# Performance work log

Measured on AMD Instinct MI355X. Metric: run time of the kernel, lower is better.

## Reference

```python
import jax, jax.numpy as jnp
import numpy as np

STRIDES = (8, 16, 32, 64, 128)
THRESHOLD = 0.5
B, C = 8, 80
HS = (160, 80, 40, 20, 10)


def setup_inputs() -> dict:
    key = jax.random.key(0)
    ks = jax.random.split(key, 3 * len(HS))
    d = {}
    for i, h in enumerate(HS):
        d[f"cls_{i}"] = jax.random.normal(ks[3 * i], (B, C, h, h), jnp.float32)
        d[f"bbox_{i}"] = jax.random.normal(ks[3 * i + 1], (B, 4, h, h), jnp.float32)
        d[f"ctr_{i}"] = jax.random.normal(ks[3 * i + 2], (B, 1, h, h), jnp.float32)
    return d


def _filter_level(cls, bbox, ctr, stride, thr):
    # cls: [B,C,H,W], bbox: [B,4,H,W], ctr: [B,1,H,W] (NCHW, as asserted in source)
    b, c, h, w = cls.shape
    scores = cls.transpose(0, 2, 3, 1).reshape(b, h * w, c)   # [B,HW,C]
    bboxes = bbox.transpose(0, 2, 3, 1).reshape(b, h * w, 4)  # [B,HW,4]
    ctrs = ctr.transpose(0, 2, 3, 1).reshape(b, h * w, 1)     # [B,HW,1]
    # FilterModule keeps locations whose max class score exceeds threshold.
    mask = (jnp.max(scores, axis=-1) > thr)[..., None].astype(scores.dtype)  # [B,HW,1]
    ys, xs = jnp.meshgrid(jnp.arange(h), jnp.arange(w), indexing="ij")
    half = stride // 2
    coord = jnp.stack([xs * stride + half, ys * stride + half], axis=-1)  # [H,W,2]
    coord = coord.reshape(h * w, 2).astype(scores.dtype)
    coord = jnp.broadcast_to(coord, (b, h * w, 2))
    # Static-shape compaction: zero out non-selected locations instead of
    # producing dynamic-length per-image lists (jit-compatible equivalent of
    # the per-image coord/score/bbox/centerness gather).
    return jnp.concatenate(
        [coord * mask, scores * mask, bboxes * mask, ctrs * mask], axis=-1
    )  # [B, HW, 2 + C + 4 + 1]


def reference(cls_0, bbox_0, ctr_0, cls_1, bbox_1, ctr_1, cls_2, bbox_2, ctr_2,
              cls_3, bbox_3, ctr_3, cls_4, bbox_4, ctr_4):
    levels = [
        (cls_0, bbox_0, ctr_0),
        (cls_1, bbox_1, ctr_1),
        (cls_2, bbox_2, ctr_2),
        (cls_3, bbox_3, ctr_3),
        (cls_4, bbox_4, ctr_4),
    ]
    return tuple(
        _filter_level(c, bb, ct, s, THRESHOLD)
        for (c, bb, ct), s in zip(levels, STRIDES)
    )
```

## Files before the change

### kernel.cpp

```cpp
#include <hip/hip_runtime.h>

#define OUTCH 87
#define WPOS  8
#define WWORDS 704

typedef float f32x4 __attribute__((ext_vector_type(4)));

__global__ __launch_bounds__(256) void fcos_filter_kernel(
    const float* __restrict__ cl0, const float* __restrict__ bb0, const float* __restrict__ ct0,
    const float* __restrict__ cl1, const float* __restrict__ bb1, const float* __restrict__ ct1,
    const float* __restrict__ cl2, const float* __restrict__ bb2, const float* __restrict__ ct2,
    const float* __restrict__ cl3, const float* __restrict__ bb3, const float* __restrict__ ct3,
    const float* __restrict__ cl4, const float* __restrict__ bb4, const float* __restrict__ ct4,
    float* __restrict__ out)
{
    __shared__ float lds[4 * WWORDS];

    const int tid  = threadIdx.x;
    const int wv   = tid >> 6;
    const int lane = tid & 63;
    float* wlds  = lds + wv * WWORDS;
    float* wflag = wlds + 696;

    const int gw = blockIdx.x * 4 + wv;

    const float *cls, *bbx, *ctr;
    int img, wi, HW, W, str, ksh;
    size_t obase;
    if (gw < 25600)      { cls=cl0;bbx=bb0;ctr=ct0;HW=25600;W=160;str=8;  ksh=4;obase=0u;
                           img = gw / 3200;          wi = gw - img * 3200; }
    else if (gw < 32000) { cls=cl1;bbx=bb1;ctr=ct1;HW=6400; W=80; str=16; ksh=3;obase=17817600u;
                           const int t = gw - 25600; img = t / 800;  wi = t - img * 800; }
    else if (gw < 33600) { cls=cl2;bbx=bb2;ctr=ct2;HW=1600; W=40; str=32; ksh=2;obase=22272000u;
                           const int t = gw - 32000; img = t / 200;  wi = t - img * 200; }
    else if (gw < 34000) { cls=cl3;bbx=bb3;ctr=ct3;HW=400;  W=20; str=64; ksh=1;obase=23385600u;
                           const int t = gw - 33600; img = t / 50;   wi = t - img * 50; }
    else                 { cls=cl4;bbx=bb4;ctr=ct4;HW=100;  W=10; str=128;ksh=0;obase=23664000u;
                           const int t = gw - 34000; img = t / 13;   wi = t - img * 13; }

    const int p0    = wi * WPOS;
    const int valid = min(WPOS, HW - p0);

    const int  cb  = lane >> 1;
    const int  q   = lane & 1;
    const bool pok = (4 * q) < valid;
    const size_t posoff = (size_t)(p0 + 4 * q);

    float4 v0, v1, v2;
    float4 fm; fm.x = fm.y = fm.z = fm.w = -1e30f;
    if (pok) {
        const float* a0 = cls + ((size_t)img * 80 + cb) * HW + posoff;
        v0 = *reinterpret_cast<const float4*>(a0);
        v1 = *reinterpret_cast<const float4*>(a0 + (size_t)32 * HW);
        fm.x = fmaxf(v0.x, v1.x); fm.y = fmaxf(v0.y, v1.y);
        fm.z = fmaxf(v0.z, v1.z); fm.w = fmaxf(v0.w, v1.w);
    }
    const bool r2 = pok && (cb < 21);
    if (r2) {
        const int c = 64 + cb;
        const float* s = (c < 80) ? cls + ((size_t)img * 80 + c) * HW
                       : (c < 84) ? bbx + ((size_t)img * 4 + (c - 80)) * HW
                                  : ctr + (size_t)img * HW;
        v2 = *reinterpret_cast<const float4*>(s + posoff);
        if (cb < 16) {
            fm.x = fmaxf(fm.x, v2.x); fm.y = fmaxf(fm.y, v2.y);
            fm.z = fmaxf(fm.z, v2.z); fm.w = fmaxf(fm.w, v2.w);
        }
    }

    #pragma unroll
    for (int m = 2; m <= 32; m <<= 1) {
        fm.x = fmaxf(fm.x, __shfl_xor(fm.x, m));
        fm.y = fmaxf(fm.y, __shfl_xor(fm.y, m));
        fm.z = fmaxf(fm.z, __shfl_xor(fm.z, m));
        fm.w = fmaxf(fm.w, __shfl_xor(fm.w, m));
    }
    float4 mk;
    mk.x = (fm.x > 0.5f) ? 1.0f : 0.0f;
    mk.y = (fm.y > 0.5f) ? 1.0f : 0.0f;
    mk.z = (fm.z > 0.5f) ? 1.0f : 0.0f;
    mk.w = (fm.w > 0.5f) ? 1.0f : 0.0f;

    const int r0w = 4 * q * 87;
    if (pok) {
        wlds[r0w +   0 + 2 + cb]      = v0.x * mk.x;
        wlds[r0w +  87 + 2 + cb]      = v0.y * mk.y;
        wlds[r0w + 174 + 2 + cb]      = v0.z * mk.z;
        wlds[r0w + 261 + 2 + cb]      = v0.w * mk.w;
        wlds[r0w +   0 + 34 + cb]     = v1.x * mk.x;
        wlds[r0w +  87 + 34 + cb]     = v1.y * mk.y;
        wlds[r0w + 174 + 34 + cb]     = v1.z * mk.z;
        wlds[r0w + 261 + 34 + cb]     = v1.w * mk.w;
    }
    if (r2) {
        wlds[r0w +   0 + 66 + cb]     = v2.x * mk.x;
        wlds[r0w +  87 + 66 + cb]     = v2.y * mk.y;
        wlds[r0w + 174 + 66 + cb]     = v2.z * mk.z;
        wlds[r0w + 261 + 66 + cb]     = v2.w * mk.w;
    }
    if (lane < 2) {
        f32x4 mo; mo.x = mk.x; mo.y = mk.y; mo.z = mk.z; mo.w = mk.w;
        *reinterpret_cast<f32x4*>(wflag + 4 * lane) = mo;
    }
    if (lane < 8) {
        const float m = wflag[lane];
        const int pg = p0 + lane;
        const int t  = pg >> ksh;
        const int y  = t / 10;
        const int x  = pg - y * W;
        wlds[lane * 87 + 0] = (float)(x * str + (str >> 1)) * m;
        wlds[lane * 87 + 1] = (float)(y * str + (str >> 1)) * m;
    }

    float* dst = out + obase + ((size_t)img * HW + p0) * OUTCH;
    const int nw = valid * OUTCH;
    {
        const int w = 4 * lane;
        if (w < nw) *reinterpret_cast<f32x4*>(dst + w) = *reinterpret_cast<const f32x4*>(wlds + w);
    }
    {
        const int w = 4 * (lane + 64);
        if (w < nw) *reinterpret_cast<f32x4*>(dst + w) = *reinterpret_cast<const f32x4*>(wlds + w);
    }
    {
        const int w = 4 * (lane + 128);
        if (w < nw) *reinterpret_cast<f32x4*>(dst + w) = *reinterpret_cast<const f32x4*>(wlds + w);
    }
}

extern "C" void kernel_launch(void* const* d_in, const int* in_sizes, int n_in,
                              void* d_out, int out_size, void* d_ws, size_t ws_size,
                              hipStream_t stream) {
    (void)in_sizes; (void)n_in; (void)out_size; (void)d_ws; (void)ws_size;
    fcos_filter_kernel<<<8526, 256, 0, stream>>>(
        (const float*)d_in[0],  (const float*)d_in[1],  (const float*)d_in[2],
        (const float*)d_in[3],  (const float*)d_in[4],  (const float*)d_in[5],
        (const float*)d_in[6],  (const float*)d_in[7],  (const float*)d_in[8],
        (const float*)d_in[9],  (const float*)d_in[10], (const float*)d_in[11],
        (const float*)d_in[12], (const float*)d_in[13], (const float*)d_in[14],
        (float*)d_out);
}
```

Measured before the change: 34.98 us.

## Make kernel persistent with grid-stride tiles and prefetch next tile's loads

Launches a fixed grid of 2048 blocks where each wave walks tiles with a grid stride. The global loads for the next tile are issued before the current tile is processed, so load latency overlaps with the LDS transpose and the stores. Loads are now unconditional, using a clamped offset for invalid positions, to keep them hoistable. This costs extra registers and leaves the last iteration with nothing to overlap, and with fewer blocks in flight memory-level parallelism may drop.

```diff
diff --git a/kernel.cpp b/kernel.cpp
--- a/kernel.cpp
+++ b/kernel.cpp
@@ -1,72 +1,69 @@
 #include <hip/hip_runtime.h>
-
-#define OUTCH 87
-#define WPOS  8
-#define WWORDS 704
 
 typedef float f32x4 __attribute__((ext_vector_type(4)));
 
-__global__ __launch_bounds__(256) void fcos_filter_kernel(
-    const float* __restrict__ cl0, const float* __restrict__ bb0, const float* __restrict__ ct0,
-    const float* __restrict__ cl1, const float* __restrict__ bb1, const float* __restrict__ ct1,
-    const float* __restrict__ cl2, const float* __restrict__ bb2, const float* __restrict__ ct2,
-    const float* __restrict__ cl3, const float* __restrict__ bb3, const float* __restrict__ ct3,
-    const float* __restrict__ cl4, const float* __restrict__ bb4, const float* __restrict__ ct4,
-    float* __restrict__ out)
+#define NTILES  34104
+#define NWAVES  8192
+#define WWORDS  704
+
+struct Tile {
+    const float *cls, *bbx, *ctr;
+    int img, HW, W, str, ksh, p0, valid;
+    long obase;
+};
+
+__device__ __forceinline__ Tile decode(int gw,
+    const float* cl0, const float* bb0, const float* ct0,
+    const float* cl1, const float* bb1, const float* ct1,
+    const float* cl2, const float* bb2, const float* ct2,
+    const float* cl3, const float* bb3, const float* ct3,
+    const float* cl4, const float* bb4, const float* ct4)
 {
-    __shared__ float lds[4 * WWORDS];
+    Tile T; int wi;
+    if (gw < 25600)      { T.cls=cl0;T.bbx=bb0;T.ctr=ct0;T.HW=25600;T.W=160;T.str=8;  T.ksh=4;T.obase=0;
+                           T.img = gw / 3200;          wi = gw - T.img * 3200; }
+    else if (gw < 32000) { T.cls=cl1;T.bbx=bb1;T.ctr=ct1;T.HW=6400; T.W=80; T.str=16; T.ksh=3;T.obase=17817600;
+                           const int u = gw - 25600;   T.img = u / 800;  wi = u - T.img * 800; }
+    else if (gw < 33600) { T.cls=cl2;T.bbx=bb2;T.ctr=ct2;T.HW=1600; T.W=40; T.str=32; T.ksh=2;T.obase=22272000;
+                           const int u = gw - 32000;   T.img = u / 200;  wi = u - T.img * 200; }
+    else if (gw < 34000) { T.cls=cl3;T.bbx=bb3;T.ctr=ct3;T.HW=400;  T.W=20; T.str=64; T.ksh=1;T.obase=23385600;
+                           const int u = gw - 33600;   T.img = u / 50;   wi = u - T.img * 50; }
+    else                 { T.cls=cl4;T.bbx=bb4;T.ctr=ct4;T.HW=100;  T.W=10; T.str=128;T.ksh=0;T.obase=23664000;
+                           const int u = gw - 34000;   T.img = u / 13;   wi = u - T.img * 13; }
+    T.p0 = wi * 8;
+    T.valid = min(8, T.HW - T.p0);
+    return T;
+}
 
-    const int tid  = threadIdx.x;
-    const int wv   = tid >> 6;
-    const int lane = tid & 63;
-    float* wlds  = lds + wv * WWORDS;
-    float* wflag = wlds + 696;
+__device__ __forceinline__ void issue(const Tile& T, int cb, int q,
+                                      float4& v0, float4& v1, float4& v2)
+{
+    const int qo = (4 * q < T.valid) ? 4 * q : 0;
+    const size_t po = (size_t)(T.p0 + qo);
+    const float* a0 = T.cls + ((size_t)T.img * 80 + cb) * T.HW + po;
+    v0 = *reinterpret_cast<const float4*>(a0);
+    v1 = *reinterpret_cast<const float4*>(a0 + (size_t)32 * T.HW);
+    const int c = 64 + ((cb < 21) ? cb : 20);
+    const float* s = (c < 80) ? T.cls + ((size_t)T.img * 80 + c) * T.HW
+                   : (c < 84) ? T.bbx + ((size_t)T.img * 4 + (c - 80)) * T.HW
+                              : T.ctr + (size_t)T.img * T.HW;
+    v2 = *reinterpret_cast<const float4*>(s + po);
+}
 
-    const int gw = blockIdx.x * 4 + wv;
+__device__ __forceinline__ void process(const Tile& T, int lane, int cb, int q,
+                                        float* wlds, float* wflag, float* __restrict__ out,
+                                        const float4& v0, const float4& v1, const float4& v2)
+{
+    const bool pok = 4 * q < T.valid;
 
-    const float *cls, *bbx, *ctr;
-    int img, wi, HW, W, str, ksh;
-    size_t obase;
-    if (gw < 25600)      { cls=cl0;bbx=bb0;ctr=ct0;HW=25600;W=160;str=8;  ksh=4;obase=0u;
-                           img = gw / 3200;          wi = gw - img * 3200; }
-    else if (gw < 32000) { cls=cl1;bbx=bb1;ctr=ct1;HW=6400; W=80; str=16; ksh=3;obase=17817600u;
-                           const int t = gw - 25600; img = t / 800;  wi = t - img * 800; }
-    else if (gw < 33600) { cls=cl2;bbx=bb2;ctr=ct2;HW=1600; W=40; str=32; ksh=2;obase=22272000u;
-                           const int t = gw - 32000; img = t / 200;  wi = t - img * 200; }
-    else if (gw < 34000) { cls=cl3;bbx=bb3;ctr=ct3;HW=400;  W=20; str=64; ksh=1;obase=23385600u;
-                           const int t = gw - 33600; img = t / 50;   wi = t - img * 50; }
-    else                 { cls=cl4;bbx=bb4;ctr=ct4;HW=100;  W=10; str=128;ksh=0;obase=23664000u;
-                           const int t = gw - 34000; img = t / 13;   wi = t - img * 13; }
-
-    const int p0    = wi * WPOS;
-    const int valid = min(WPOS, HW - p0);
-
-    const int  cb  = lane >> 1;
-    const int  q   = lane & 1;
-    const bool pok = (4 * q) < valid;
-    const size_t posoff = (size_t)(p0 + 4 * q);
-
-    float4 v0, v1, v2;
-    float4 fm; fm.x = fm.y = fm.z = fm.w = -1e30f;
-    if (pok) {
-        const float* a0 = cls + ((size_t)img * 80 + cb) * HW + posoff;
-        v0 = *reinterpret_cast<const float4*>(a0);
-        v1 = *reinterpret_cast<const float4*>(a0 + (size_t)32 * HW);
-        fm.x = fmaxf(v0.x, v1.x); fm.y = fmaxf(v0.y, v1.y);
-        fm.z = fmaxf(v0.z, v1.z); fm.w = fmaxf(v0.w, v1.w);
+    float4 fm;
+    fm.x = fmaxf(v0.x, v1.x); fm.y = fmaxf(v0.y, v1.y);
+    fm.z = fmaxf(v0.z, v1.z); fm.w = fmaxf(v0.w, v1.w);
+    if (cb < 16) {
+        fm.x = fmaxf(fm.x, v2.x); fm.y = fmaxf(fm.y, v2.y);
+        fm.z = fmaxf(fm.z, v2.z); fm.w = fmaxf(fm.w, v2.w);
     }
-    const bool r2 = pok && (cb < 21);
-    if (r2) {
-        const int c = 64 + cb;
-        const float* s = (c < 80) ? cls + ((size_t)img * 80 + c) * HW
-                       : (c < 84) ? bbx + ((size_t)img * 4 + (c - 80)) * HW
-                                  : ctr + (size_t)img * HW;
-        v2 = *reinterpret_cast<const float4*>(s + posoff);
-        if (cb < 16) {
-            fm.x = fmaxf(fm.x, v2.x); fm.y = fmaxf(fm.y, v2.y);
-            fm.z = fmaxf(fm.z, v2.z); fm.w = fmaxf(fm.w, v2.w);
-        }
-    }
+    if (!pok) { fm.x = fm.y = fm.z = fm.w = -1e30f; }
 
     #pragma unroll
     for (int m = 2; m <= 32; m <<= 1) {
@@ -83,20 +80,20 @@
 
     const int r0w = 4 * q * 87;
     if (pok) {
-        wlds[r0w +   0 + 2 + cb]      = v0.x * mk.x;
-        wlds[r0w +  87 + 2 + cb]      = v0.y * mk.y;
-        wlds[r0w + 174 + 2 + cb]      = v0.z * mk.z;
-        wlds[r0w + 261 + 2 + cb]      = v0.w * mk.w;
-        wlds[r0w +   0 + 34 + cb]     = v1.x * mk.x;
-        wlds[r0w +  87 + 34 + cb]     = v1.y * mk.y;
-        wlds[r0w + 174 + 34 + cb]     = v1.z * mk.z;
-        wlds[r0w + 261 + 34 + cb]     = v1.w * mk.w;
-    }
-    if (r2) {
-        wlds[r0w +   0 + 66 + cb]     = v2.x * mk.x;
-        wlds[r0w +  87 + 66 + cb]     = v2.y * mk.y;
-        wlds[r0w + 174 + 66 + cb]     = v2.z * mk.z;
-        wlds[r0w + 261 + 66 + cb]     = v2.w * mk.w;
+        wlds[r0w +   0 + 2 + cb]  = v0.x * mk.x;
+        wlds[r0w +  87 + 2 + cb]  = v0.y * mk.y;
+        wlds[r0w + 174 + 2 + cb]  = v0.z * mk.z;
+        wlds[r0w + 261 + 2 + cb]  = v0.w * mk.w;
+        wlds[r0w +   0 + 34 + cb] = v1.x * mk.x;
+        wlds[r0w +  87 + 34 + cb] = v1.y * mk.y;
+        wlds[r0w + 174 + 34 + cb] = v1.z * mk.z;
+        wlds[r0w + 261 + 34 + cb] = v1.w * mk.w;
+        if (cb < 21) {
+            wlds[r0w +   0 + 66 + cb] = v2.x * mk.x;
+            wlds[r0w +  87 + 66 + cb] = v2.y * mk.y;
+            wlds[r0w + 174 + 66 + cb] = v2.z * mk.z;
+            wlds[r0w + 261 + 66 + cb] = v2.w * mk.w;
+        }
     }
     if (lane < 2) {
         f32x4 mo; mo.x = mk.x; mo.y = mk.y; mo.z = mk.z; mo.w = mk.w;
@@ -104,16 +101,16 @@
     }
     if (lane < 8) {
         const float m = wflag[lane];
-        const int pg = p0 + lane;
-        const int t  = pg >> ksh;
-        const int y  = t / 10;
-        const int x  = pg - y * W;
-        wlds[lane * 87 + 0] = (float)(x * str + (str >> 1)) * m;
-        wlds[lane * 87 + 1] = (float)(y * str + (str >> 1)) * m;
+        const int pg = T.p0 + lane;
+        const int tt = pg >> T.ksh;
+        const int y  = tt / 10;
+        const int x  = pg - y * T.W;
+        wlds[lane * 87 + 0] = (float)(x * T.str + (T.str >> 1)) * m;
+        wlds[lane * 87 + 1] = (float)(y * T.str + (T.str >> 1)) * m;
     }
 
-    float* dst = out + obase + ((size_t)img * HW + p0) * OUTCH;
-    const int nw = valid * OUTCH;
+    float* dst = out + T.obase + ((size_t)T.img * T.HW + T.p0) * 87;
+    const int nw = T.valid * 87;
     {
         const int w = 4 * lane;
         if (w < nw) *reinterpret_cast<f32x4*>(dst + w) = *reinterpret_cast<const f32x4*>(wlds + w);
@@ -128,11 +125,49 @@
     }
 }
 
+__global__ __launch_bounds__(256) void fcos_filter_kernel(
+    const float* __restrict__ cl0, const float* __restrict__ bb0, const float* __restrict__ ct0,
+    const float* __restrict__ cl1, const float* __restrict__ bb1, const float* __restrict__ ct1,
+    const float* __restrict__ cl2, const float* __restrict__ bb2, const float* __restrict__ ct2,
+    const float* __restrict__ cl3, const float* __restrict__ bb3, const float* __restrict__ ct3,
+    const float* __restrict__ cl4, const float* __restrict__ bb4, const float* __restrict__ ct4,
+    float* __restrict__ out)
+{
+    __shared__ float lds[4 * WWORDS];
+    const int tid  = threadIdx.x;
+    const int lane = tid & 63;
+    float* wlds  = lds + (tid >> 6) * WWORDS;
+    float* wflag = wlds + 696;
+    const int cb = lane >> 1;
+    const int q  = lane & 1;
+
+    int t = __builtin_amdgcn_readfirstlane((int)(blockIdx.x * 4) + (tid >> 6));
+
+    Tile cur = decode(t, cl0,bb0,ct0, cl1,bb1,ct1, cl2,bb2,ct2, cl3,bb3,ct3, cl4,bb4,ct4);
+    float4 a0, a1, a2;
+    issue(cur, cb, q, a0, a1, a2);
+
+    while (true) {
+        const int tn = t + NWAVES;
+        if (tn < NTILES) {
+            Tile nxt = decode(tn, cl0,bb0,ct0, cl1,bb1,ct1, cl2,bb2,ct2, cl3,bb3,ct3, cl4,bb4,ct4);
+            float4 b0, b1, b2;
+            issue(nxt, cb, q, b0, b1, b2);
+            process(cur, lane, cb, q, wlds, wflag, out, a0, a1, a2);
+            cur = nxt; a0 = b0; a1 = b1; a2 = b2;
+            t = tn;
+        } else {
+            process(cur, lane, cb, q, wlds, wflag, out, a0, a1, a2);
+            break;
+        }
+    }
+}
+
 extern "C" void kernel_launch(void* const* d_in, const int* in_sizes, int n_in,
                               void* d_out, int out_size, void* d_ws, size_t ws_size,
                               hipStream_t stream) {
     (void)in_sizes; (void)n_in; (void)out_size; (void)d_ws; (void)ws_size;
-    fcos_filter_kernel<<<8526, 256, 0, stream>>>(
+    fcos_filter_kernel<<<2048, 256, 0, stream>>>(
         (const float*)d_in[0],  (const float*)d_in[1],  (const float*)d_in[2],
         (const float*)d_in[3],  (const float*)d_in[4],  (const float*)d_in[5],
         (const float*)d_in[6],  (const float*)d_in[7],  (const float*)d_in[8],
```

Measured after the change: 37.97 us. +8.5%, slower.
